# Kernel optimization log

Measured on AMD Instinct MI355X. Metric: run time of the kernel, lower is better.

Reference implementation:

```python
import jax, jax.numpy as jnp
import numpy as np

L_LAYERS, B, N, K, D, H, FFN, NCLS = 6, 4, 23890, 1024, 256, 8, 1024, 15
SPATIAL = np.array([[134, 134], [67, 67], [34, 34], [17, 17]], dtype=np.int32)


def setup_inputs() -> dict:
    key = jax.random.key(0)
    ks = jax.random.split(key, 32)
    inp = {}
    inp["query"] = jax.random.normal(ks[0], (B, N, D), jnp.float32)
    inp["query_pos"] = jax.random.normal(ks[1], (B, N, D), jnp.float32)
    inp["spatial_shapes"] = jnp.asarray(SPATIAL, jnp.int32)
    lsi = np.concatenate([[0], np.cumsum(SPATIAL[:, 0] * SPATIAL[:, 1])[:-1]])
    inp["level_start_index"] = jnp.asarray(lsi, jnp.int32)
    inp["valid_ratios"] = jnp.ones((B, 4, 2), jnp.float32)
    inp["query_key_padding_mask"] = jnp.zeros((B, N), jnp.bool_)
    inp["foreground_score"] = jax.random.uniform(ks[2], (B, N), jnp.float32)
    inp["focus_token_nums"] = jax.random.randint(ks[3], (B,), 1, K + 1, jnp.int32)
    # unique per-row foreground indices (Focus-DETR uses top-k indices)
    pk = jax.random.split(ks[4], L_LAYERS * B)
    inds = jax.vmap(lambda k_: jax.random.permutation(k_, N)[:K])(pk)
    inp["foreground_inds"] = inds.reshape(L_LAYERS, B, K).astype(jnp.int32)
    s = 0.02
    def mat(k_, shape):
        return jax.random.normal(k_, shape, jnp.float32) * s
    inp["Wq"] = mat(ks[5], (L_LAYERS, D, D)); inp["bq"] = jnp.zeros((L_LAYERS, D))
    inp["Wk"] = mat(ks[6], (L_LAYERS, D, D)); inp["bk"] = jnp.zeros((L_LAYERS, D))
    inp["Wv"] = mat(ks[7], (L_LAYERS, D, D)); inp["bv"] = jnp.zeros((L_LAYERS, D))
    inp["Wo"] = mat(ks[8], (L_LAYERS, D, D)); inp["bo"] = jnp.zeros((L_LAYERS, D))
    inp["ln1_g"] = jnp.ones((L_LAYERS, D)); inp["ln1_b"] = jnp.zeros((L_LAYERS, D))
    inp["W1"] = mat(ks[9], (L_LAYERS, D, FFN)); inp["b1"] = jnp.zeros((L_LAYERS, FFN))
    inp["W2"] = mat(ks[10], (L_LAYERS, FFN, D)); inp["b2"] = jnp.zeros((L_LAYERS, D))
    inp["ln2_g"] = jnp.ones((L_LAYERS, D)); inp["ln2_b"] = jnp.zeros((L_LAYERS, D))
    inp["W_cls"] = mat(ks[11], (D, NCLS)); inp["b_cls"] = jnp.zeros((NCLS,))
    return inp


def _layer_norm(x, g, b, eps=1e-5):
    mu = jnp.mean(x, -1, keepdims=True)
    var = jnp.mean(jnp.square(x - mu), -1, keepdims=True)
    return (x - mu) * jax.lax.rsqrt(var + eps) * g + b


def _get_reference_points(spatial_shapes, valid_ratios):
    ss = np.asarray(spatial_shapes)  # static multi-scale shapes
    refs = []
    for lvl, (h, w) in enumerate(ss):
        h, w = int(h), int(w)
        ry, rx = jnp.meshgrid(jnp.linspace(0.5, h - 0.5, h, dtype=jnp.float32),
                              jnp.linspace(0.5, w - 0.5, w, dtype=jnp.float32), indexing='ij')
        ry = ry.reshape(-1)[None] / (valid_ratios[:, None, lvl, 1] * h)
        rx = rx.reshape(-1)[None] / (valid_ratios[:, None, lvl, 0] * w)
        refs.append(jnp.stack((rx, ry), -1))  # [B, h*w, 2]
    rp = jnp.concatenate(refs, 1)            # [B, N, 2]
    return rp[:, :, None] * valid_ratios[:, None]  # [B, N, n_lvl, 2]


def reference(query, spatial_shapes, level_start_index, valid_ratios, query_pos,
              query_key_padding_mask, foreground_score, focus_token_nums, foreground_inds,
              Wq, bq, Wk, bk, Wv, bv, Wo, bo, ln1_g, ln1_b, W1, b1, W2, b2,
              ln2_g, ln2_b, W_cls, b_cls):
    b, n, d = query.shape
    nh = H
    hd = d // nh
    rp = _get_reference_points(spatial_shapes, valid_ratios)  # [B,N,S,2]
    s, p = rp.shape[2], rp.shape[3]
    rp_flat = rp.reshape(b, n, s * p)
    output = query
    num_layers = foreground_inds.shape[0]
    k = foreground_inds.shape[-1]
    pos_mask = jnp.arange(k, dtype=focus_token_nums.dtype)[None, :]  # [1,K]
    for l in range(num_layers):
        inds = foreground_inds[l]                                       # [B,K]
        q = jnp.take_along_axis(output, inds[..., None], axis=1)        # [B,K,D]
        qp = jnp.take_along_axis(query_pos, inds[..., None], axis=1)    # [B,K,D]
        fg = jnp.take_along_axis(foreground_score, inds, axis=1)        # [B,K]
        _ = jnp.take_along_axis(rp_flat, inds[..., None], axis=1).reshape(b, k, s, p)
        # enhanced MCSP score modulation
        score_tgt = q @ W_cls + b_cls                                   # [B,K,15]
        mc = jnp.max(jax.nn.sigmoid(score_tgt), -1) * fg                # [B,K]
        tgt = q * mc[..., None]
        qk = tgt + qp
        Q = (qk @ Wq[l] + bq[l]).reshape(b, k, nh, hd)
        Kt = (qk @ Wk[l] + bk[l]).reshape(b, k, nh, hd)
        V = (tgt @ Wv[l] + bv[l]).reshape(b, k, nh, hd)
        attn = jax.nn.softmax(jnp.einsum('bqhd,bkhd->bhqk', Q, Kt) / np.sqrt(hd), axis=-1)
        o = jnp.einsum('bhqk,bkhd->bqhd', attn, V).reshape(b, k, d) @ Wo[l] + bo[l]
        x = _layer_norm(tgt + o, ln1_g[l], ln1_b[l])
        ff = jax.nn.relu(x @ W1[l] + b1[l]) @ W2[l] + b2[l]
        q_new = _layer_norm(x + ff, ln2_g[l], ln2_b[l])                 # [B,K,D]
        # ragged scatter-back: only first focus_token_nums[i] rows per batch item
        valid = pos_mask < focus_token_nums[:, None]                    # [B,K]
        safe = jnp.where(valid, inds, n)                                # OOB -> dropped
        output = jax.vmap(lambda o_, i_, v_: o_.at[i_].set(v_, mode='drop'))(output, safe, q_new)
    return output
```

## Files before the change

kernel.cpp:

```cpp
#include <hip/hip_runtime.h>
#include <math.h>

#define LAYERS 6
#define BB 4
#define NN 23890
#define KTOK 1024
#define DD 256
#define NH 8
#define HDIM 32
#define FFND 1024
#define NCLS 15
#define MROWS (BB*KTOK)

typedef __attribute__((ext_vector_type(8))) short bf16x8;
typedef __attribute__((ext_vector_type(4))) float f32x4;

__device__ __forceinline__ unsigned short f2bf(float x) {
    unsigned u = __float_as_uint(x);
    u += 0x7fffu + ((u >> 16) & 1u);
    return (unsigned short)(u >> 16);
}

__device__ __forceinline__ float block_sum256(float v) {
    __shared__ float sh[4];
    #pragma unroll
    for (int o = 32; o; o >>= 1) v += __shfl_xor(v, o);
    const int lane = threadIdx.x & 63, w = threadIdx.x >> 6;
    __syncthreads();
    if (lane == 0) sh[w] = v;
    __syncthreads();
    return sh[0] + sh[1] + sh[2] + sh[3];
}

__global__ __launch_bounds__(256) void transpose_cast_k(
    const float* __restrict__ W, unsigned short* __restrict__ Wt,
    int Kd, int Nd)
{
    __shared__ float tile[32][33];
    const int n0 = blockIdx.x * 32, k0 = blockIdx.y * 32;
    const size_t loff = (size_t)blockIdx.z * Kd * Nd;
    const int t = threadIdx.x;
    const int r = t >> 3, c = (t & 7) * 4;
    const float4 v = *(const float4*)&W[loff + (size_t)(k0 + r) * Nd + n0 + c];
    tile[r][c + 0] = v.x; tile[r][c + 1] = v.y;
    tile[r][c + 2] = v.z; tile[r][c + 3] = v.w;
    __syncthreads();
    ushort4 p;
    p.x = f2bf(tile[c + 0][r]);
    p.y = f2bf(tile[c + 1][r]);
    p.z = f2bf(tile[c + 2][r]);
    p.w = f2bf(tile[c + 3][r]);
    *(ushort4*)&Wt[loff + (size_t)(n0 + r) * Kd + k0 + c] = p;
}

__global__ __launch_bounds__(256) void gather_k(
    const float* __restrict__ outp, const float* __restrict__ qpos,
    const float* __restrict__ fg, const int* __restrict__ inds,
    const float* __restrict__ Wcls, const float* __restrict__ bcls,
    float* __restrict__ tgt, unsigned short* __restrict__ tgt_bf,
    unsigned short* __restrict__ qk_bf)
{
    const int row = blockIdx.x, t = threadIdx.x;
    const int b = row >> 10;
    const int k = row & 1023;
    const int ind = inds[b * KTOK + k];
    __shared__ float qs[DD];
    __shared__ float sco[NCLS];
    __shared__ float mcsh;
    const size_t src = ((size_t)b * NN + ind) * DD + t;
    const float qv = outp[src];
    qs[t] = qv;
    __syncthreads();
    if (t < NCLS) {
        float s = bcls[t];
        #pragma unroll 8
        for (int d = 0; d < DD; ++d) s = fmaf(qs[d], Wcls[d * NCLS + t], s);
        sco[t] = s;
    }
    __syncthreads();
    if (t == 0) {
        float m = sco[0];
        #pragma unroll
        for (int j = 1; j < NCLS; ++j) m = fmaxf(m, sco[j]);
        mcsh = fg[(size_t)b * NN + ind] / (1.0f + expf(-m));
    }
    __syncthreads();
    const float tv = qv * mcsh;
    const size_t off = (size_t)row * DD + t;
    tgt[off] = tv;
    tgt_bf[off] = f2bf(tv);
    qk_bf[off] = f2bf(tv + qpos[src]);
}

__device__ __forceinline__ void mgemm_body(
    const unsigned short* __restrict__ A, const unsigned short* __restrict__ Wt,
    const float* __restrict__ bias, float* __restrict__ Cf,
    unsigned short* __restrict__ Cb, unsigned short* __restrict__ VtO,
    int Nsz, int Ksz, bool relu, int bm, int bn)
{
    __shared__ unsigned short As[64 * 32];
    __shared__ unsigned short Bs[64 * 32];
    const int t = threadIdx.x;
    const int lane = t & 63, wave = t >> 6;
    const int ln15 = lane & 15, kg = lane >> 4;
    const int wm = (wave >> 1) * 32, wn = (wave & 1) * 32;
    const int sr = t >> 2, sc = (t & 3) * 8;

    f32x4 acc[2][2];
    #pragma unroll
    for (int i = 0; i < 2; ++i)
        #pragma unroll
        for (int j = 0; j < 2; ++j) acc[i][j] = (f32x4)0.0f;

    for (int k0 = 0; k0 < Ksz; k0 += 32) {
        *(bf16x8*)&As[sr * 32 + sc] =
            *(const bf16x8*)&A[(size_t)(bm + sr) * Ksz + k0 + sc];
        *(bf16x8*)&Bs[sr * 32 + sc] =
            *(const bf16x8*)&Wt[(size_t)(bn + sr) * Ksz + k0 + sc];
        __syncthreads();
        const bf16x8 a0 = *(const bf16x8*)&As[(wm + ln15) * 32 + kg * 8];
        const bf16x8 a1 = *(const bf16x8*)&As[(wm + 16 + ln15) * 32 + kg * 8];
        const bf16x8 b0 = *(const bf16x8*)&Bs[(wn + ln15) * 32 + kg * 8];
        const bf16x8 b1 = *(const bf16x8*)&Bs[(wn + 16 + ln15) * 32 + kg * 8];
        acc[0][0] = __builtin_amdgcn_mfma_f32_16x16x32_bf16(a0, b0, acc[0][0], 0, 0, 0);
        acc[0][1] = __builtin_amdgcn_mfma_f32_16x16x32_bf16(a0, b1, acc[0][1], 0, 0, 0);
        acc[1][0] = __builtin_amdgcn_mfma_f32_16x16x32_bf16(a1, b0, acc[1][0], 0, 0, 0);
        acc[1][1] = __builtin_amdgcn_mfma_f32_16x16x32_bf16(a1, b1, acc[1][1], 0, 0, 0);
        __syncthreads();
    }

    #pragma unroll
    for (int mt = 0; mt < 2; ++mt) {
        #pragma unroll
        for (int nt = 0; nt < 2; ++nt) {
            const int col = bn + wn + nt * 16 + ln15;
            const int r0  = bm + wm + mt * 16 + kg * 4;
            const float bv = bias[col];
            if (VtO) {
                const int bidx = r0 >> 10, tok0 = r0 & 1023;
                const int hh = col >> 5, dd = col & 31;
                ushort4 pk;
                pk.x = f2bf(acc[mt][nt][0] + bv);
                pk.y = f2bf(acc[mt][nt][1] + bv);
                pk.z = f2bf(acc[mt][nt][2] + bv);
                pk.w = f2bf(acc[mt][nt][3] + bv);
                *(ushort4*)&VtO[(((size_t)bidx * NH + hh) * HDIM + dd) * KTOK + tok0] = pk;
            } else {
                #pragma unroll
                for (int j = 0; j < 4; ++j) {
                    float v = acc[mt][nt][j] + bv;
                    if (relu) v = fmaxf(v, 0.0f);
                    const size_t o = (size_t)(r0 + j) * Nsz + col;
                    if (Cf) Cf[o] = v;
                    if (Cb) Cb[o] = f2bf(v);
                }
            }
        }
    }
}

__global__ __launch_bounds__(256) void mgemm_k(
    const unsigned short* __restrict__ A, const unsigned short* __restrict__ Wt,
    const float* __restrict__ bias, float* __restrict__ Cf,
    unsigned short* __restrict__ Cb, int Nsz, int Ksz, int relu)
{
    mgemm_body(A, Wt, bias, Cf, Cb, nullptr, Nsz, Ksz, relu != 0,
               blockIdx.y * 64, blockIdx.x * 64);
}

__global__ __launch_bounds__(256) void mgemm_qkv_k(
    const unsigned short* __restrict__ qk_bf, const unsigned short* __restrict__ tgt_bf,
    const unsigned short* __restrict__ wqt, const float* __restrict__ bq,
    const unsigned short* __restrict__ wkt, const float* __restrict__ bk,
    const unsigned short* __restrict__ wvt, const float* __restrict__ bv,
    unsigned short* __restrict__ Qbf, unsigned short* __restrict__ Kbf,
    unsigned short* __restrict__ Vtg)
{
    const unsigned short* A; const unsigned short* W; const float* bi;
    unsigned short* Cb = nullptr; unsigned short* Vt = nullptr;
    if (blockIdx.z == 0)      { A = qk_bf;  W = wqt; bi = bq; Cb = Qbf; }
    else if (blockIdx.z == 1) { A = qk_bf;  W = wkt; bi = bk; Cb = Kbf; }
    else                      { A = tgt_bf; W = wvt; bi = bv; Vt = Vtg; }
    mgemm_body(A, W, bi, nullptr, Cb, Vt, DD, DD, false,
               blockIdx.y * 64, blockIdx.x * 64);
}

#define ATT_PSTR 68

__global__ __launch_bounds__(256) void attn_mfma_k(
    const unsigned short* __restrict__ Qbf, const unsigned short* __restrict__ Kbf,
    const unsigned short* __restrict__ Vtg, unsigned short* __restrict__ Ob)
{
    const int qt = blockIdx.x, h = blockIdx.y, b = blockIdx.z;
    const int t = threadIdx.x;
    const int w = t >> 6, lane = t & 63;
    const int ln15 = lane & 15, kg = lane >> 4;

    __shared__ unsigned short Ks[64 * 32];
    __shared__ unsigned short Vts[32 * 64];
    __shared__ float Ps[4][16 * ATT_PSTR];

    const int q0 = qt * 64 + w * 16;
    const bf16x8 aQ = *(const bf16x8*)
        &Qbf[((size_t)(b * KTOK + q0 + ln15)) * DD + h * HDIM + kg * 8];

    f32x4 accO[2];
    accO[0] = (f32x4)0.0f; accO[1] = (f32x4)0.0f;
    float m_i[4], l_i[4];
    #pragma unroll
    for (int i = 0; i < 4; ++i) { m_i[i] = -1e30f; l_i[i] = 0.0f; }
    const float scale = 0.17677669529663687f;

    const int krow = t >> 2, kd0 = (t & 3) * 8;
    const int vd = t >> 3, vt0 = (t & 7) * 8;

    for (int kt = 0; kt < 16; ++kt) {
        __syncthreads();
        *(bf16x8*)&Ks[krow * 32 + kd0] = *(const bf16x8*)
            &Kbf[((size_t)(b * KTOK + kt * 64 + krow)) * DD + h * HDIM + kd0];
        *(bf16x8*)&Vts[vd * 64 + vt0] = *(const bf16x8*)
            &Vtg[(((size_t)b * NH + h) * HDIM + vd) * KTOK + kt * 64 + vt0];
        __syncthreads();

        f32x4 s[4];
        #pragma unroll
        for (int st = 0; st < 4; ++st) {
            const bf16x8 bK = *(const bf16x8*)&Ks[(st * 16 + ln15) * 32 + kg * 8];
            s[st] = __builtin_amdgcn_mfma_f32_16x16x32_bf16(aQ, bK, (f32x4)0.0f, 0, 0, 0);
        }
        #pragma unroll
        for (int r = 0; r < 4; ++r) {
            float v0 = s[0][r] * scale, v1 = s[1][r] * scale;
            float v2 = s[2][r] * scale, v3 = s[3][r] * scale;
            float rm = fmaxf(fmaxf(v0, v1), fmaxf(v2, v3));
            rm = fmaxf(rm, __shfl_xor(rm, 1));
            rm = fmaxf(rm, __shfl_xor(rm, 2));
            rm = fmaxf(rm, __shfl_xor(rm, 4));
            rm = fmaxf(rm, __shfl_xor(rm, 8));
            const float mnew = fmaxf(m_i[r], rm);
            const float alpha = __expf(m_i[r] - mnew);
            v0 = __expf(v0 - mnew); v1 = __expf(v1 - mnew);
            v2 = __expf(v2 - mnew); v3 = __expf(v3 - mnew);
            float ls = v0 + v1 + v2 + v3;
            ls += __shfl_xor(ls, 1); ls += __shfl_xor(ls, 2);
            ls += __shfl_xor(ls, 4); ls += __shfl_xor(ls, 8);
            l_i[r] = l_i[r] * alpha + ls;
            m_i[r] = mnew;
            accO[0][r] *= alpha; accO[1][r] *= alpha;
            const int pr = (kg * 4 + r) * ATT_PSTR + ln15;
            Ps[w][pr +  0] = v0;
            Ps[w][pr + 16] = v1;
            Ps[w][pr + 32] = v2;
            Ps[w][pr + 48] = v3;
        }
        #pragma unroll
        for (int kc = 0; kc < 2; ++kc) {
            const float* prow = &Ps[w][ln15 * ATT_PSTR + kc * 32 + kg * 8];
            const float4 pa = *(const float4*)prow;
            const float4 pb = *(const float4*)(prow + 4);
            bf16x8 aP;
            aP[0] = (short)f2bf(pa.x); aP[1] = (short)f2bf(pa.y);
            aP[2] = (short)f2bf(pa.z); aP[3] = (short)f2bf(pa.w);
            aP[4] = (short)f2bf(pb.x); aP[5] = (short)f2bf(pb.y);
            aP[6] = (short)f2bf(pb.z); aP[7] = (short)f2bf(pb.w);
            #pragma unroll
            for (int dt = 0; dt < 2; ++dt) {
                const bf16x8 bV = *(const bf16x8*)
                    &Vts[(dt * 16 + ln15) * 64 + kc * 32 + kg * 8];
                accO[dt] = __builtin_amdgcn_mfma_f32_16x16x32_bf16(aP, bV, accO[dt], 0, 0, 0);
            }
        }
    }

    #pragma unroll
    for (int dt = 0; dt < 2; ++dt)
        #pragma unroll
        for (int r = 0; r < 4; ++r) {
            const float v = accO[dt][r] / l_i[r];
            Ob[((size_t)(b * KTOK + q0 + kg * 4 + r)) * DD + h * HDIM + dt * 16 + ln15]
                = f2bf(v);
        }
}

__global__ __launch_bounds__(256) void add_ln_k(
    const float* __restrict__ A, const float* __restrict__ Bv,
    const float* __restrict__ g, const float* __restrict__ be,
    float* __restrict__ outp, unsigned short* __restrict__ outp_bf)
{
    const int row = blockIdx.x, t = threadIdx.x;
    const size_t off = (size_t)row * DD + t;
    const float v = A[off] + Bv[off];
    const float mu = block_sum256(v) * (1.0f / DD);
    const float d = v - mu;
    const float var = block_sum256(d * d) * (1.0f / DD);
    const float r = d * rsqrtf(var + 1e-5f) * g[t] + be[t];
    outp[off] = r;
    outp_bf[off] = f2bf(r);
}

__global__ __launch_bounds__(256) void ln_scatter_k(
    const float* __restrict__ X, const float* __restrict__ F,
    const float* __restrict__ g, const float* __restrict__ be,
    const int* __restrict__ inds, const int* __restrict__ focus,
    float* __restrict__ outp)
{
    const int row = blockIdx.x, t = threadIdx.x;
    const int b = row >> 10;
    const int k = row & 1023;
    if (k >= focus[b]) return;
    const size_t off = (size_t)row * DD + t;
    const float v = X[off] + F[off];
    const float mu = block_sum256(v) * (1.0f / DD);
    const float d = v - mu;
    const float var = block_sum256(d * d) * (1.0f / DD);
    const int ind = inds[b * KTOK + k];
    outp[((size_t)b * NN + ind) * DD + t] = d * rsqrtf(var + 1e-5f) * g[t] + be[t];
}

extern "C" void kernel_launch(void* const* d_in, const int* in_sizes, int n_in,
                              void* d_out, int out_size, void* d_ws, size_t ws_size,
                              hipStream_t stream)
{
    const float* query = (const float*)d_in[0];
    const float* qpos  = (const float*)d_in[1];
    const float* fg    = (const float*)d_in[6];
    const int*   focus = (const int*)d_in[7];
    const int*   finds = (const int*)d_in[8];
    const float* Wq = (const float*)d_in[9];  const float* bq = (const float*)d_in[10];
    const float* Wk = (const float*)d_in[11]; const float* bk = (const float*)d_in[12];
    const float* Wv = (const float*)d_in[13]; const float* bv = (const float*)d_in[14];
    const float* Wo = (const float*)d_in[15]; const float* bo = (const float*)d_in[16];
    const float* g1 = (const float*)d_in[17]; const float* be1 = (const float*)d_in[18];
    const float* W1 = (const float*)d_in[19]; const float* b1 = (const float*)d_in[20];
    const float* W2 = (const float*)d_in[21]; const float* b2 = (const float*)d_in[22];
    const float* g2 = (const float*)d_in[23]; const float* be2 = (const float*)d_in[24];
    const float* Wcls = (const float*)d_in[25]; const float* bcls = (const float*)d_in[26];
    float* out = (float*)d_out;

    char* p = (char*)d_ws;
    const size_t MD4 = (size_t)MROWS * DD * 4;
    const size_t MD2 = (size_t)MROWS * DD * 2;
    float* tgt  = (float*)p;  p += MD4;
    float* olin = (float*)p;  p += MD4;
    float* x    = (float*)p;  p += MD4;
    float* ff2  = (float*)p;  p += MD4;
    unsigned short* tgt_bf   = (unsigned short*)p;  p += MD2;
    unsigned short* qk_bf    = (unsigned short*)p;  p += MD2;
    unsigned short* attno_bf = (unsigned short*)p;  p += MD2;
    unsigned short* x_bf     = (unsigned short*)p;  p += MD2;
    unsigned short* Qbf      = (unsigned short*)p;  p += MD2;
    unsigned short* Kbf      = (unsigned short*)p;  p += MD2;
    unsigned short* Vtg      = (unsigned short*)p;  p += MD2;
    unsigned short* ff1_bf   = (unsigned short*)p;  p += (size_t)MROWS * FFND * 2;
    const size_t WSQ = (size_t)LAYERS * DD * DD;
    const size_t WFF = (size_t)LAYERS * DD * FFND;
    unsigned short* wqt = (unsigned short*)p;  p += WSQ * 2;
    unsigned short* wkt = (unsigned short*)p;  p += WSQ * 2;
    unsigned short* wvt = (unsigned short*)p;  p += WSQ * 2;
    unsigned short* wot = (unsigned short*)p;  p += WSQ * 2;
    unsigned short* w1t = (unsigned short*)p;  p += WFF * 2;
    unsigned short* w2t = (unsigned short*)p;  p += WFF * 2;

    transpose_cast_k<<<dim3(DD / 32, DD / 32, LAYERS), 256, 0, stream>>>(Wq, wqt, DD, DD);
    transpose_cast_k<<<dim3(DD / 32, DD / 32, LAYERS), 256, 0, stream>>>(Wk, wkt, DD, DD);
    transpose_cast_k<<<dim3(DD / 32, DD / 32, LAYERS), 256, 0, stream>>>(Wv, wvt, DD, DD);
    transpose_cast_k<<<dim3(DD / 32, DD / 32, LAYERS), 256, 0, stream>>>(Wo, wot, DD, DD);
    transpose_cast_k<<<dim3(FFND / 32, DD / 32, LAYERS), 256, 0, stream>>>(W1, w1t, DD, FFND);
    transpose_cast_k<<<dim3(DD / 32, FFND / 32, LAYERS), 256, 0, stream>>>(W2, w2t, FFND, DD);

    hipMemcpyAsync(out, query, (size_t)BB * NN * DD * sizeof(float),
                   hipMemcpyDeviceToDevice, stream);

    for (int l = 0; l < LAYERS; ++l) {
        const int* inds = finds + (size_t)l * BB * KTOK;
        gather_k<<<MROWS, 256, 0, stream>>>(out, qpos, fg, inds, Wcls, bcls,
                                            tgt, tgt_bf, qk_bf);
        mgemm_qkv_k<<<dim3(DD / 64, MROWS / 64, 3), 256, 0, stream>>>(
            qk_bf, tgt_bf,
            wqt + (size_t)l * DD * DD, bq + (size_t)l * DD,
            wkt + (size_t)l * DD * DD, bk + (size_t)l * DD,
            wvt + (size_t)l * DD * DD, bv + (size_t)l * DD,
            Qbf, Kbf, Vtg);
        attn_mfma_k<<<dim3(KTOK / 64, NH, BB), 256, 0, stream>>>(Qbf, Kbf, Vtg, attno_bf);
        mgemm_k<<<dim3(DD / 64, MROWS / 64), 256, 0, stream>>>(
            attno_bf, wot + (size_t)l * DD * DD, bo + (size_t)l * DD,
            olin, nullptr, DD, DD, 0);
        add_ln_k<<<MROWS, 256, 0, stream>>>(tgt, olin,
            g1 + (size_t)l * DD, be1 + (size_t)l * DD, x, x_bf);
        mgemm_k<<<dim3(FFND / 64, MROWS / 64), 256, 0, stream>>>(
            x_bf, w1t + (size_t)l * DD * FFND, b1 + (size_t)l * FFND,
            nullptr, ff1_bf, FFND, DD, 1);
        mgemm_k<<<dim3(DD / 64, MROWS / 64), 256, 0, stream>>>(
            ff1_bf, w2t + (size_t)l * DD * FFND, b2 + (size_t)l * DD,
            ff2, nullptr, DD, FFND, 0);
        ln_scatter_k<<<MROWS, 256, 0, stream>>>(x, ff2,
            g2 + (size_t)l * DD, be2 + (size_t)l * DD, inds, focus, out);
    }
    (void)in_sizes; (void)n_in; (void)out_size; (void)ws_size;
}
```

Before: 958.0 us.

## Fuse output-projection and FFN2 GEMMs with residual LayerNorm and scatter

Replaces the separate Wo GEMM plus add_ln kernel, and the W2 GEMM plus ln_scatter kernel, with full-row-width GEMM kernels. Each block computes 32 rows by all 256 columns, adds bias and residual, reduces mean and variance in registers and shared memory, and writes the normalized (and scattered) result directly. This removes the fp32 intermediate round-trips and two launches per layer. It also merges the four square-weight transposes into one launch and replaces hipMemcpyAsync with a copy kernel. The trade-offs are only 128 blocks per fused GEMM, which may underfill the GPU, and a one-pass variance (E[x²]−μ²) that is numerically less stable.

```diff
diff --git a/kernel.cpp b/kernel.cpp
--- a/kernel.cpp
+++ b/kernel.cpp
@@ -21,15 +21,41 @@
     return (unsigned short)(u >> 16);
 }
 
-__device__ __forceinline__ float block_sum256(float v) {
-    __shared__ float sh[4];
-    #pragma unroll
-    for (int o = 32; o; o >>= 1) v += __shfl_xor(v, o);
-    const int lane = threadIdx.x & 63, w = threadIdx.x >> 6;
-    __syncthreads();
-    if (lane == 0) sh[w] = v;
-    __syncthreads();
-    return sh[0] + sh[1] + sh[2] + sh[3];
+__global__ __launch_bounds__(256) void copy_k(
+    const float4* __restrict__ src, float4* __restrict__ dst, int n4)
+{
+    int i = blockIdx.x * 256 + threadIdx.x;
+    const int stride = gridDim.x * 256;
+    for (; i < n4; i += stride) dst[i] = src[i];
+}
+
+__global__ __launch_bounds__(256) void transpose_sq_k(
+    const float* __restrict__ Wq, const float* __restrict__ Wk,
+    const float* __restrict__ Wv, const float* __restrict__ Wo,
+    unsigned short* __restrict__ wqt, unsigned short* __restrict__ wkt,
+    unsigned short* __restrict__ wvt, unsigned short* __restrict__ wot)
+{
+    __shared__ float tile[32][33];
+    const int l = blockIdx.z >> 2, sel = blockIdx.z & 3;
+    const float* W; unsigned short* Wt;
+    if (sel == 0)      { W = Wq; Wt = wqt; }
+    else if (sel == 1) { W = Wk; Wt = wkt; }
+    else if (sel == 2) { W = Wv; Wt = wvt; }
+    else               { W = Wo; Wt = wot; }
+    const int n0 = blockIdx.x * 32, k0 = blockIdx.y * 32;
+    const size_t loff = (size_t)l * DD * DD;
+    const int t = threadIdx.x;
+    const int r = t >> 3, c = (t & 7) * 4;
+    const float4 v = *(const float4*)&W[loff + (size_t)(k0 + r) * DD + n0 + c];
+    tile[r][c + 0] = v.x; tile[r][c + 1] = v.y;
+    tile[r][c + 2] = v.z; tile[r][c + 3] = v.w;
+    __syncthreads();
+    ushort4 p;
+    p.x = f2bf(tile[c + 0][r]);
+    p.y = f2bf(tile[c + 1][r]);
+    p.z = f2bf(tile[c + 2][r]);
+    p.w = f2bf(tile[c + 3][r]);
+    *(ushort4*)&Wt[loff + (size_t)(n0 + r) * DD + k0 + c] = p;
 }
 
 __global__ __launch_bounds__(256) void transpose_cast_k(
@@ -282,39 +308,157 @@
         }
 }
 
-__global__ __launch_bounds__(256) void add_ln_k(
-    const float* __restrict__ A, const float* __restrict__ Bv,
+__device__ __forceinline__ void wide_gemm_ln(
+    const unsigned short* __restrict__ A, const unsigned short* __restrict__ Wt,
+    const float* __restrict__ bias, const float* __restrict__ res,
     const float* __restrict__ g, const float* __restrict__ be,
-    float* __restrict__ outp, unsigned short* __restrict__ outp_bf)
-{
-    const int row = blockIdx.x, t = threadIdx.x;
-    const size_t off = (size_t)row * DD + t;
-    const float v = A[off] + Bv[off];
-    const float mu = block_sum256(v) * (1.0f / DD);
-    const float d = v - mu;
-    const float var = block_sum256(d * d) * (1.0f / DD);
-    const float r = d * rsqrtf(var + 1e-5f) * g[t] + be[t];
-    outp[off] = r;
-    outp_bf[off] = f2bf(r);
-}
-
-__global__ __launch_bounds__(256) void ln_scatter_k(
-    const float* __restrict__ X, const float* __restrict__ F,
-    const float* __restrict__ g, const float* __restrict__ be,
+    int Ksz, int bm,
+    float* __restrict__ xo, unsigned short* __restrict__ xo_bf,
     const int* __restrict__ inds, const int* __restrict__ focus,
     float* __restrict__ outp)
 {
-    const int row = blockIdx.x, t = threadIdx.x;
-    const int b = row >> 10;
-    const int k = row & 1023;
-    if (k >= focus[b]) return;
-    const size_t off = (size_t)row * DD + t;
-    const float v = X[off] + F[off];
-    const float mu = block_sum256(v) * (1.0f / DD);
-    const float d = v - mu;
-    const float var = block_sum256(d * d) * (1.0f / DD);
-    const int ind = inds[b * KTOK + k];
-    outp[((size_t)b * NN + ind) * DD + t] = d * rsqrtf(var + 1e-5f) * g[t] + be[t];
+    __shared__ unsigned short As[32 * 32];
+    __shared__ unsigned short Bs[256 * 32];
+    __shared__ float redS[4][32], redQ[4][32];
+    __shared__ float mu_s[32], rs_s[32];
+
+    const int t = threadIdx.x;
+    const int lane = t & 63, w = t >> 6;
+    const int ln15 = lane & 15, kg = lane >> 4;
+    const int wn = w * 64;
+    const int sr4 = t >> 2, sc4 = (t & 3) * 8;
+
+    f32x4 acc[2][4];
+    #pragma unroll
+    for (int i = 0; i < 2; ++i)
+        #pragma unroll
+        for (int j = 0; j < 4; ++j) acc[i][j] = (f32x4)0.0f;
+
+    for (int k0 = 0; k0 < Ksz; k0 += 32) {
+        if (t < 128)
+            *(bf16x8*)&As[(t >> 2) * 32 + (t & 3) * 8] =
+                *(const bf16x8*)&A[(size_t)(bm + (t >> 2)) * Ksz + k0 + (t & 3) * 8];
+        #pragma unroll
+        for (int rep = 0; rep < 4; ++rep) {
+            const int rrow = rep * 64 + sr4;
+            *(bf16x8*)&Bs[rrow * 32 + sc4] =
+                *(const bf16x8*)&Wt[(size_t)rrow * Ksz + k0 + sc4];
+        }
+        __syncthreads();
+        const bf16x8 a0 = *(const bf16x8*)&As[ln15 * 32 + kg * 8];
+        const bf16x8 a1 = *(const bf16x8*)&As[(16 + ln15) * 32 + kg * 8];
+        #pragma unroll
+        for (int nt = 0; nt < 4; ++nt) {
+            const bf16x8 bf = *(const bf16x8*)&Bs[(wn + nt * 16 + ln15) * 32 + kg * 8];
+            acc[0][nt] = __builtin_amdgcn_mfma_f32_16x16x32_bf16(a0, bf, acc[0][nt], 0, 0, 0);
+            acc[1][nt] = __builtin_amdgcn_mfma_f32_16x16x32_bf16(a1, bf, acc[1][nt], 0, 0, 0);
+        }
+        __syncthreads();
+    }
+
+    float s1[2][4], s2[2][4];
+    #pragma unroll
+    for (int mt = 0; mt < 2; ++mt)
+        #pragma unroll
+        for (int j = 0; j < 4; ++j) { s1[mt][j] = 0.0f; s2[mt][j] = 0.0f; }
+
+    #pragma unroll
+    for (int mt = 0; mt < 2; ++mt) {
+        #pragma unroll
+        for (int nt = 0; nt < 4; ++nt) {
+            const int col = wn + nt * 16 + ln15;
+            const float bv = bias[col];
+            #pragma unroll
+            for (int j = 0; j < 4; ++j) {
+                const int rl = mt * 16 + kg * 4 + j;
+                float v = acc[mt][nt][j] + bv + res[(size_t)(bm + rl) * DD + col];
+                acc[mt][nt][j] = v;
+                s1[mt][j] += v;
+                s2[mt][j] += v * v;
+            }
+        }
+    }
+    #pragma unroll
+    for (int mt = 0; mt < 2; ++mt)
+        #pragma unroll
+        for (int j = 0; j < 4; ++j) {
+            float a = s1[mt][j], q = s2[mt][j];
+            a += __shfl_xor(a, 1); q += __shfl_xor(q, 1);
+            a += __shfl_xor(a, 2); q += __shfl_xor(q, 2);
+            a += __shfl_xor(a, 4); q += __shfl_xor(q, 4);
+            a += __shfl_xor(a, 8); q += __shfl_xor(q, 8);
+            if (ln15 == 0) {
+                const int rl = mt * 16 + kg * 4 + j;
+                redS[w][rl] = a; redQ[w][rl] = q;
+            }
+        }
+    __syncthreads();
+    if (t < 32) {
+        const float a = redS[0][t] + redS[1][t] + redS[2][t] + redS[3][t];
+        const float q = redQ[0][t] + redQ[1][t] + redQ[2][t] + redQ[3][t];
+        const float mu = a * (1.0f / DD);
+        const float var = q * (1.0f / DD) - mu * mu;
+        mu_s[t] = mu;
+        rs_s[t] = rsqrtf(var + 1e-5f);
+    }
+    __syncthreads();
+
+    if (outp == nullptr) {
+        #pragma unroll
+        for (int mt = 0; mt < 2; ++mt)
+            #pragma unroll
+            for (int nt = 0; nt < 4; ++nt) {
+                const int col = wn + nt * 16 + ln15;
+                const float gv = g[col], bev = be[col];
+                #pragma unroll
+                for (int j = 0; j < 4; ++j) {
+                    const int rl = mt * 16 + kg * 4 + j;
+                    const float r = (acc[mt][nt][j] - mu_s[rl]) * rs_s[rl] * gv + bev;
+                    const size_t o = (size_t)(bm + rl) * DD + col;
+                    xo[o] = r;
+                    xo_bf[o] = f2bf(r);
+                }
+            }
+    } else {
+        const int bidx = bm >> 10;
+        const int focusb = focus[bidx];
+        #pragma unroll
+        for (int mt = 0; mt < 2; ++mt)
+            #pragma unroll
+            for (int j = 0; j < 4; ++j) {
+                const int rl = mt * 16 + kg * 4 + j;
+                const int kk = (bm & 1023) + rl;
+                if (kk >= focusb) continue;
+                const int ind = inds[bidx * KTOK + kk];
+                float* orow = &outp[((size_t)bidx * NN + ind) * DD];
+                #pragma unroll
+                for (int nt = 0; nt < 4; ++nt) {
+                    const int col = wn + nt * 16 + ln15;
+                    orow[col] = (acc[mt][nt][j] - mu_s[rl]) * rs_s[rl] * g[col] + be[col];
+                }
+            }
+    }
+}
+
+__global__ __launch_bounds__(256) void oproj_ln_k(
+    const unsigned short* __restrict__ attno_bf, const unsigned short* __restrict__ wot,
+    const float* __restrict__ bo, const float* __restrict__ tgt,
+    const float* __restrict__ g1, const float* __restrict__ be1,
+    float* __restrict__ x, unsigned short* __restrict__ x_bf)
+{
+    wide_gemm_ln(attno_bf, wot, bo, tgt, g1, be1, DD, blockIdx.x * 32,
+                 x, x_bf, nullptr, nullptr, nullptr);
+}
+
+__global__ __launch_bounds__(256) void ffn2_ln_scatter_k(
+    const unsigned short* __restrict__ ff1_bf, const unsigned short* __restrict__ w2t,
+    const float* __restrict__ b2, const float* __restrict__ x,
+    const float* __restrict__ g2, const float* __restrict__ be2,
+    const int* __restrict__ inds, const int* __restrict__ focus,
+    float* __restrict__ outp)
+{
+    wide_gemm_ln(ff1_bf, w2t, b2, x, g2, be2, FFND, blockIdx.x * 32,
+                 nullptr, nullptr, inds, focus, outp);
 }
 
 extern "C" void kernel_launch(void* const* d_in, const int* in_sizes, int n_in,
@@ -341,9 +485,7 @@
     const size_t MD4 = (size_t)MROWS * DD * 4;
     const size_t MD2 = (size_t)MROWS * DD * 2;
     float* tgt  = (float*)p;  p += MD4;
-    float* olin = (float*)p;  p += MD4;
     float* x    = (float*)p;  p += MD4;
-    float* ff2  = (float*)p;  p += MD4;
     unsigned short* tgt_bf   = (unsigned short*)p;  p += MD2;
     unsigned short* qk_bf    = (unsigned short*)p;  p += MD2;
     unsigned short* attno_bf = (unsigned short*)p;  p += MD2;
@@ -361,15 +503,13 @@
     unsigned short* w1t = (unsigned short*)p;  p += WFF * 2;
     unsigned short* w2t = (unsigned short*)p;  p += WFF * 2;
 
-    transpose_cast_k<<<dim3(DD / 32, DD / 32, LAYERS), 256, 0, stream>>>(Wq, wqt, DD, DD);
-    transpose_cast_k<<<dim3(DD / 32, DD / 32, LAYERS), 256, 0, stream>>>(Wk, wkt, DD, DD);
-    transpose_cast_k<<<dim3(DD / 32, DD / 32, LAYERS), 256, 0, stream>>>(Wv, wvt, DD, DD);
-    transpose_cast_k<<<dim3(DD / 32, DD / 32, LAYERS), 256, 0, stream>>>(Wo, wot, DD, DD);
+    transpose_sq_k<<<dim3(DD / 32, DD / 32, LAYERS * 4), 256, 0, stream>>>(
+        Wq, Wk, Wv, Wo, wqt, wkt, wvt, wot);
     transpose_cast_k<<<dim3(FFND / 32, DD / 32, LAYERS), 256, 0, stream>>>(W1, w1t, DD, FFND);
     transpose_cast_k<<<dim3(DD / 32, FFND / 32, LAYERS), 256, 0, stream>>>(W2, w2t, FFND, DD);
 
-    hipMemcpyAsync(out, query, (size_t)BB * NN * DD * sizeof(float),
-                   hipMemcpyDeviceToDevice, stream);
+    copy_k<<<2048, 256, 0, stream>>>((const float4*)query, (float4*)out,
+                                     (int)((size_t)BB * NN * DD / 4));
 
     for (int l = 0; l < LAYERS; ++l) {
         const int* inds = finds + (size_t)l * BB * KTOK;
@@ -382,19 +522,15 @@
             wvt + (size_t)l * DD * DD, bv + (size_t)l * DD,
             Qbf, Kbf, Vtg);
         attn_mfma_k<<<dim3(KTOK / 64, NH, BB), 256, 0, stream>>>(Qbf, Kbf, Vtg, attno_bf);
-        mgemm_k<<<dim3(DD / 64, MROWS / 64), 256, 0, stream>>>(
+        oproj_ln_k<<<MROWS / 32, 256, 0, stream>>>(
             attno_bf, wot + (size_t)l * DD * DD, bo + (size_t)l * DD,
-            olin, nullptr, DD, DD, 0);
-        add_ln_k<<<MROWS, 256, 0, stream>>>(tgt, olin,
-            g1 + (size_t)l * DD, be1 + (size_t)l * DD, x, x_bf);
+            tgt, g1 + (size_t)l * DD, be1 + (size_t)l * DD, x, x_bf);
         mgemm_k<<<dim3(FFND / 64, MROWS / 64), 256, 0, stream>>>(
             x_bf, w1t + (size_t)l * DD * FFND, b1 + (size_t)l * FFND,
             nullptr, ff1_bf, FFND, DD, 1);
-        mgemm_k<<<dim3(DD / 64, MROWS / 64), 256, 0, stream>>>(
+        ffn2_ln_scatter_k<<<MROWS / 32, 256, 0, stream>>>(
             ff1_bf, w2t + (size_t)l * DD * FFND, b2 + (size_t)l * DD,
-            ff2, nullptr, DD, FFND, 0);
-        ln_scatter_k<<<MROWS, 256, 0, stream>>>(x, ff2,
-            g2 + (size_t)l * DD, be2 + (size_t)l * DD, inds, focus, out);
+            x, g2 + (size_t)l * DD, be2 + (size_t)l * DD, inds, focus, out);
     }
     (void)in_sizes; (void)n_in; (void)out_size; (void)ws_size;
 }
```

Result: slower. 986.3 us (+3.0%).
